# Optimization experiments

Hardware: AMD Instinct MI355X
Metric: run time of the kernel (lower is better)

## Reference

```python
import jax, jax.numpy as jnp
import numpy as np

D_MODEL = 1024
D_HIDDEN = 4096
NUM_BANKS = 16
NUM_SELECTED = 2


def setup_inputs() -> dict:
    key = jax.random.key(0)
    ks = jax.random.split(key, 7)
    s = 0.02
    return {
        "tensor": jax.random.normal(ks[0], (4, 1024, D_MODEL), dtype=jnp.float32),
        "Wr": jax.random.normal(ks[1], (D_MODEL, NUM_BANKS), dtype=jnp.float32) * s,
        "br": jnp.zeros((NUM_BANKS,), dtype=jnp.float32),
        "W1": jax.random.normal(ks[2], (NUM_BANKS, D_MODEL, D_HIDDEN), dtype=jnp.float32) * s,
        "b1": jnp.zeros((NUM_BANKS, D_HIDDEN), dtype=jnp.float32),
        "W2": jax.random.normal(ks[3], (NUM_BANKS, D_HIDDEN, D_MODEL), dtype=jnp.float32) * s,
        "b2": jnp.zeros((NUM_BANKS, D_MODEL), dtype=jnp.float32),
    }


def reference(tensor, Wr, br, W1, b1, W2, b2):
    # Router: softmax over banks, keep top-k probabilities (BankSelector)
    logits = jnp.einsum("bsd,de->bse", tensor, Wr) + br          # [B,S,E]
    probs = jax.nn.softmax(logits, axis=-1)
    topv, topi = jax.lax.top_k(probs, NUM_SELECTED)              # [B,S,K]
    # Dense gate [B,S,E]: selected banks carry their router probability,
    # all other banks are zeroed (equivalent to sparse dispatch/combine).
    gate = jnp.sum(jax.nn.one_hot(topi, NUM_BANKS, dtype=tensor.dtype)
                   * topv[..., None], axis=-2)                    # [B,S,E]
    # Banked expert FFN (BankedLinear x2 with ReLU between)
    h = jax.nn.relu(jnp.einsum("bsd,edh->bseh", tensor, W1) + b1)  # [B,S,E,Dh]
    y = jnp.einsum("bseh,ehm->bsem", h, W2) + b2                   # [B,S,E,Dm]
    # Weighted combine across selected banks
    out = jnp.einsum("bse,bsem->bsm", gate, y)                     # [B,S,Dm]
    return out
```

## Files before the change

### kernel.cpp

```cpp
#include <hip/hip_runtime.h>
#include <stdint.h>

#define D_MODEL   1024
#define D_HIDDEN  4096
#define NBANKS    16
#define NTOK      4096

#define BM 128
#define BN 128
#define BK 32
#define TBUF (BM * BK)
#define KS2 4
#define MAXT 512

typedef __attribute__((ext_vector_type(8))) short bf16x8;
typedef __attribute__((ext_vector_type(4))) float f32x4;
typedef __attribute__((ext_vector_type(4))) unsigned int u32x4;
typedef __attribute__((ext_vector_type(2))) unsigned int u32x2;

__device__ __forceinline__ unsigned short f2bf(float f) {
  unsigned u = __builtin_bit_cast(unsigned, f);
  u += 0x7FFFu + ((u >> 16) & 1u);
  return (unsigned short)(u >> 16);
}

__device__ __forceinline__ unsigned cvtpk(float lo, float hi) {
  unsigned r;
  asm("v_cvt_pk_bf16_f32 %0, %1, %2" : "=v"(r) : "v"(lo), "v"(hi));
  return r;
}

__device__ __forceinline__ void lds_barrier() {
  asm volatile("s_waitcnt lgkmcnt(0)" ::: "memory");
  __builtin_amdgcn_sched_barrier(0);
  __builtin_amdgcn_s_barrier();
  __builtin_amdgcn_sched_barrier(0);
}

__device__ __forceinline__ int sidx(int r, int k) {
  return (r << 5) + ((((k >> 3) ^ ((r >> 1) & 3)) << 3) | (k & 7));
}

__global__ __launch_bounds__(256) void zero_out_k(float4* __restrict__ out4,
                                                  int* __restrict__ counts) {
  size_t i = (size_t)blockIdx.x * 256 + threadIdx.x;
  out4[i] = make_float4(0.f, 0.f, 0.f, 0.f);
  if (blockIdx.x == 0 && threadIdx.x < NBANKS) counts[threadIdx.x] = 0;
}

__global__ __launch_bounds__(256) void cvtx_k(const float* __restrict__ X,
                                              unsigned short* __restrict__ Xb) {
  const size_t i = ((size_t)blockIdx.x * 256 + threadIdx.x) * 8;
  const float4 a = *(const float4*)(X + i);
  const float4 b = *(const float4*)(X + i + 4);
  u32x4 v;
  v[0] = cvtpk(a.x, a.y); v[1] = cvtpk(a.z, a.w);
  v[2] = cvtpk(b.x, b.y); v[3] = cvtpk(b.z, b.w);
  *(u32x4*)(Xb + i) = v;
}

__global__ __launch_bounds__(64) void router_k(const float* __restrict__ x,
                                               const float* __restrict__ Wr,
                                               const float* __restrict__ br,
                                               int* __restrict__ topIdx,
                                               float* __restrict__ topGate) {
  const int t = blockIdx.x;
  const int l = threadIdx.x;
  const float* xr = x + (size_t)t * D_MODEL;

  float acc[NBANKS];
#pragma unroll
  for (int e = 0; e < NBANKS; ++e) acc[e] = 0.f;

  for (int d = l; d < D_MODEL; d += 64) {
    const float xv = xr[d];
    const float* wrow = Wr + (size_t)d * NBANKS;
#pragma unroll
    for (int e = 0; e < NBANKS; ++e) acc[e] += xv * wrow[e];
  }
#pragma unroll
  for (int e = 0; e < NBANKS; ++e) {
#pragma unroll
    for (int m = 1; m < 64; m <<= 1) acc[e] += __shfl_xor(acc[e], m, 64);
  }
#pragma unroll
  for (int e = 0; e < NBANKS; ++e) acc[e] += br[e];

  if (l == 0) {
    float mx = acc[0];
#pragma unroll
    for (int e = 1; e < NBANKS; ++e) mx = fmaxf(mx, acc[e]);
    float p[NBANKS];
    float s = 0.f;
#pragma unroll
    for (int e = 0; e < NBANKS; ++e) { p[e] = expf(acc[e] - mx); s += p[e]; }
    int i0 = 0; float v0 = p[0];
#pragma unroll
    for (int e = 1; e < NBANKS; ++e) if (p[e] > v0) { v0 = p[e]; i0 = e; }
    int i1 = -1; float v1 = -1.f;
#pragma unroll
    for (int e = 0; e < NBANKS; ++e) if (e != i0 && p[e] > v1) { v1 = p[e]; i1 = e; }
    const float inv = 1.f / s;
    topIdx[2 * t]     = i0;
    topIdx[2 * t + 1] = i1;
    topGate[2 * t]     = v0 * inv;
    topGate[2 * t + 1] = v1 * inv;
  }
}

__global__ __launch_bounds__(256) void build_lists_k(const int* __restrict__ topIdx,
                                                     const float* __restrict__ topGate,
                                                     int* __restrict__ counts,
                                                     int* __restrict__ rowlist,
                                                     float* __restrict__ gatelist) {
  const int t = blockIdx.x * 256 + threadIdx.x;
  if (t >= NTOK) return;
#pragma unroll
  for (int k = 0; k < 2; ++k) {
    const int e = topIdx[2 * t + k];
    const int p = atomicAdd(&counts[e], 1);
    rowlist[e * NTOK + p]  = t;
    gatelist[e * NTOK + p] = topGate[2 * t + k];
  }
}

__global__ void scan_k(const int* __restrict__ counts, int* __restrict__ bankOff,
                       int* __restrict__ tileE, int* __restrict__ tileM,
                       int* __restrict__ nT) {
  if (threadIdx.x == 0) {
    int s = 0;
    int t = 0;
    for (int e = 0; e < NBANKS; ++e) {
      bankOff[e] = s;
      const int c = counts[e];
      s += c;
      for (int m = 0; m < c; m += BM) {
        tileE[t] = e;
        tileM[t] = m;
        ++t;
      }
    }
    bankOff[NBANKS] = s;
    nT[0] = t;
  }
}

__global__ __launch_bounds__(256, 2) void gemm1_k(const unsigned short* __restrict__ Xb,
                                                  const float* __restrict__ W1,
                                                  const float* __restrict__ b1,
                                                  const int* __restrict__ counts,
                                                  const int* __restrict__ bankOff,
                                                  const int* __restrict__ rowlist,
                                                  const int* __restrict__ tileE,
                                                  const int* __restrict__ tileM,
                                                  const int* __restrict__ nT,
                                                  unsigned short* __restrict__ H) {
  const int tI = blockIdx.y;
  if (tI >= nT[0]) return;
  const int e   = tileE[tI];
  const int m0  = tileM[tI];
  const int cnt = counts[e];
  const int n0  = blockIdx.x * BN;

  const int tid  = threadIdx.x;
  const int lane = tid & 63;
  const int w    = tid >> 6;
  const int wm   = (w >> 1) * 64;
  const int wn   = (w & 1) * 64;

  __shared__ unsigned short Xs[2 * TBUF];
  __shared__ unsigned short Ws[2 * TBUF];

  const int arow = tid >> 1;
  const int ak   = (tid & 1) * 16;
  const int gi   = min(m0 + arow, cnt - 1);
  const int tok  = rowlist[e * NTOK + gi];
  const unsigned short* Asrc = Xb + (size_t)tok * D_MODEL + ak;
  const int xo0 = sidx(arow, ak);
  const int xo1 = sidx(arow, ak + 8);

  const int n4 = 4 * (tid & 31);
  const int k4 = 4 * (tid >> 5);
  const float* Bsrc = W1 + (size_t)e * D_MODEL * D_HIDDEN + (size_t)k4 * D_HIDDEN + n0 + n4;
  int wo[4];
#pragma unroll
  for (int i = 0; i < 4; ++i) wo[i] = sidx(n4 + i, k4);

  const int fr = lane & 15;
  const int fc = (lane >> 4) * 8;
  int aoff[4], boff[4];
#pragma unroll
  for (int i = 0; i < 4; ++i) {
    aoff[i] = sidx(wm + i * 16 + fr, fc);
    boff[i] = sidx(wn + i * 16 + fr, fc);
  }

  bf16x8 pa0, pa1, qa0, qa1;
  float pb[4][4], qb[4][4];

  f32x4 acc[4][4];
#pragma unroll
  for (int i = 0; i < 4; ++i)
#pragma unroll
    for (int j = 0; j < 4; ++j)
#pragma unroll
      for (int r = 0; r < 4; ++r) acc[i][j][r] = 0.f;

  unsigned short* xc = &Xs[0];       unsigned short* wc = &Ws[0];
  unsigned short* xn = &Xs[TBUF];    unsigned short* wn_ = &Ws[TBUF];

  auto LOADP = [&](int t) {
    const unsigned short* ap = Asrc + t * BK;
    pa0 = *(const bf16x8*)(ap);
    pa1 = *(const bf16x8*)(ap + 8);
    const float* bp = Bsrc + (size_t)t * BK * D_HIDDEN;
#pragma unroll
    for (int kk = 0; kk < 4; ++kk)
      *(float4*)&pb[kk][0] = *(const float4*)(bp + (size_t)kk * D_HIDDEN);
  };
  auto LOADQ = [&](int t) {
    const unsigned short* ap = Asrc + t * BK;
    qa0 = *(const bf16x8*)(ap);
    qa1 = *(const bf16x8*)(ap + 8);
    const float* bp = Bsrc + (size_t)t * BK * D_HIDDEN;
#pragma unroll
    for (int kk = 0; kk < 4; ++kk)
      *(float4*)&qb[kk][0] = *(const float4*)(bp + (size_t)kk * D_HIDDEN);
  };
  auto WRITEP = [&](unsigned short* xs, unsigned short* ws) {
    *(bf16x8*)(xs + xo0) = pa0;
    *(bf16x8*)(xs + xo1) = pa1;
#pragma unroll
    for (int i = 0; i < 4; ++i) {
      u32x2 v;
      v[0] = cvtpk(pb[0][i], pb[1][i]);
      v[1] = cvtpk(pb[2][i], pb[3][i]);
      *(u32x2*)(ws + wo[i]) = v;
    }
  };
  auto WRITEQ = [&](unsigned short* xs, unsigned short* ws) {
    *(bf16x8*)(xs + xo0) = qa0;
    *(bf16x8*)(xs + xo1) = qa1;
#pragma unroll
    for (int i = 0; i < 4; ++i) {
      u32x2 v;
      v[0] = cvtpk(qb[0][i], qb[1][i]);
      v[1] = cvtpk(qb[2][i], qb[3][i]);
      *(u32x2*)(ws + wo[i]) = v;
    }
  };
  auto COMPUTE = [&](const unsigned short* xs, const unsigned short* ws) {
    bf16x8 af[4], bb[4];
#pragma unroll
    for (int mb = 0; mb < 4; ++mb) af[mb] = *(const bf16x8*)(xs + aoff[mb]);
#pragma unroll
    for (int nb = 0; nb < 4; ++nb) bb[nb] = *(const bf16x8*)(ws + boff[nb]);
#pragma unroll
    for (int mb = 0; mb < 4; ++mb)
#pragma unroll
      for (int nb = 0; nb < 4; ++nb)
        acc[mb][nb] = __builtin_amdgcn_mfma_f32_16x16x32_bf16(af[mb], bb[nb], acc[mb][nb], 0, 0, 0);
  };

  const int NT = D_MODEL / BK;
  LOADP(0);
  LOADQ(1);
  WRITEP(xc, wc);
  lds_barrier();
#pragma unroll 1
  for (int t = 0; t < NT; t += 2) {
    if (t + 2 < NT) LOADP(t + 2);
    __builtin_amdgcn_sched_barrier(0);
    COMPUTE(xc, wc);
    WRITEQ(xn, wn_);
    lds_barrier();
    if (t + 3 < NT) LOADQ(t + 3);
    __builtin_amdgcn_sched_barrier(0);
    COMPUTE(xn, wn_);
    if (t + 2 < NT) WRITEP(xc, wc);
    lds_barrier();
  }

  const int hb = bankOff[e] + m0;
  const int rq = (lane >> 4) * 4;
#pragma unroll
  for (int nb = 0; nb < 4; ++nb) {
    const int col = n0 + wn + nb * 16 + fr;
    const float bias = b1[e * D_HIDDEN + col];
#pragma unroll
    for (int mb = 0; mb < 4; ++mb)
#pragma unroll
      for (int r = 0; r < 4; ++r) {
        const int rowT = wm + mb * 16 + rq + r;
        if (m0 + rowT < cnt) {
          float v = acc[mb][nb][r] + bias;
          v = fmaxf(v, 0.f);
          H[(size_t)(hb + rowT) * D_HIDDEN + col] = f2bf(v);
        }
      }
  }
}

__global__ __launch_bounds__(256, 2) void gemm2_k(const unsigned short* __restrict__ H,
                                                  const float* __restrict__ W2,
                                                  const float* __restrict__ b2,
                                                  const int* __restrict__ counts,
                                                  const int* __restrict__ bankOff,
                                                  const int* __restrict__ rowlist,
                                                  const float* __restrict__ gatelist,
                                                  const int* __restrict__ tileE,
                                                  const int* __restrict__ tileM,
                                                  const int* __restrict__ nT,
                                                  float* __restrict__ out) {
  const int tI = blockIdx.y >> 2;
  const int kc = blockIdx.y & 3;
  if (tI >= nT[0]) return;
  const int e   = tileE[tI];
  const int m0  = tileM[tI];
  const int cnt = counts[e];
  const int n0  = blockIdx.x * BN;
  const int kc0 = kc * (D_HIDDEN / KS2);

  const int tid  = threadIdx.x;
  const int lane = tid & 63;
  const int w    = tid >> 6;
  const int wm   = (w >> 1) * 64;
  const int wn   = (w & 1) * 64;

  __shared__ unsigned short Xs[2 * TBUF];
  __shared__ unsigned short Ws[2 * TBUF];

  const int arow = tid >> 1;
  const int ak   = (tid & 1) * 16;
  const int hb   = bankOff[e];
  const int gi   = hb + min(m0 + arow, cnt - 1);
  const unsigned short* Asrc = H + (size_t)gi * D_HIDDEN + kc0 + ak;
  const int xo0 = sidx(arow, ak);
  const int xo1 = sidx(arow, ak + 8);

  const int n4 = 4 * (tid & 31);
  const int k4 = 4 * (tid >> 5);
  const float* Bsrc = W2 + (size_t)e * D_HIDDEN * D_MODEL + (size_t)(kc0 + k4) * D_MODEL + n0 + n4;
  int wo[4];
#pragma unroll
  for (int i = 0; i < 4; ++i) wo[i] = sidx(n4 + i, k4);

  const int fr = lane & 15;
  const int fc = (lane >> 4) * 8;
  int aoff[4], boff[4];
#pragma unroll
  for (int i = 0; i < 4; ++i) {
    aoff[i] = sidx(wm + i * 16 + fr, fc);
    boff[i] = sidx(wn + i * 16 + fr, fc);
  }

  bf16x8 pa0, pa1, qa0, qa1;
  float pb[4][4], qb[4][4];

  f32x4 acc[4][4];
#pragma unroll
  for (int i = 0; i < 4; ++i)
#pragma unroll
    for (int j = 0; j < 4; ++j)
#pragma unroll
      for (int r = 0; r < 4; ++r) acc[i][j][r] = 0.f;

  unsigned short* xc = &Xs[0];       unsigned short* wc = &Ws[0];
  unsigned short* xn = &Xs[TBUF];    unsigned short* wn_ = &Ws[TBUF];

  auto LOADP = [&](int t) {
    const unsigned short* ap = Asrc + t * BK;
    pa0 = *(const bf16x8*)(ap);
    pa1 = *(const bf16x8*)(ap + 8);
    const float* bp = Bsrc + (size_t)t * BK * D_MODEL;
#pragma unroll
    for (int kk = 0; kk < 4; ++kk)
      *(float4*)&pb[kk][0] = *(const float4*)(bp + (size_t)kk * D_MODEL);
  };
  auto LOADQ = [&](int t) {
    const unsigned short* ap = Asrc + t * BK;
    qa0 = *(const bf16x8*)(ap);
    qa1 = *(const bf16x8*)(ap + 8);
    const float* bp = Bsrc + (size_t)t * BK * D_MODEL;
#pragma unroll
    for (int kk = 0; kk < 4; ++kk)
      *(float4*)&qb[kk][0] = *(const float4*)(bp + (size_t)kk * D_MODEL);
  };
  auto WRITEP = [&](unsigned short* xs, unsigned short* ws) {
    *(bf16x8*)(xs + xo0) = pa0;
    *(bf16x8*)(xs + xo1) = pa1;
#pragma unroll
    for (int i = 0; i < 4; ++i) {
      u32x2 v;
      v[0] = cvtpk(pb[0][i], pb[1][i]);
      v[1] = cvtpk(pb[2][i], pb[3][i]);
      *(u32x2*)(ws + wo[i]) = v;
    }
  };
  auto WRITEQ = [&](unsigned short* xs, unsigned short* ws) {
    *(bf16x8*)(xs + xo0) = qa0;
    *(bf16x8*)(xs + xo1) = qa1;
#pragma unroll
    for (int i = 0; i < 4; ++i) {
      u32x2 v;
      v[0] = cvtpk(qb[0][i], qb[1][i]);
      v[1] = cvtpk(qb[2][i], qb[3][i]);
      *(u32x2*)(ws + wo[i]) = v;
    }
  };
  auto COMPUTE = [&](const unsigned short* xs, const unsigned short* ws) {
    bf16x8 af[4], bb[4];
#pragma unroll
    for (int mb = 0; mb < 4; ++mb) af[mb] = *(const bf16x8*)(xs + aoff[mb]);
#pragma unroll
    for (int nb = 0; nb < 4; ++nb) bb[nb] = *(const bf16x8*)(ws + boff[nb]);
#pragma unroll
    for (int mb = 0; mb < 4; ++mb)
#pragma unroll
      for (int nb = 0; nb < 4; ++nb)
        acc[mb][nb] = __builtin_amdgcn_mfma_f32_16x16x32_bf16(af[mb], bb[nb], acc[mb][nb], 0, 0, 0);
  };

  const int NT = (D_HIDDEN / KS2) / BK;
  LOADP(0);
  LOADQ(1);
  WRITEP(xc, wc);
  lds_barrier();
#pragma unroll 1
  for (int t = 0; t < NT; t += 2) {
    if (t + 2 < NT) LOADP(t + 2);
    __builtin_amdgcn_sched_barrier(0);
    COMPUTE(xc, wc);
    WRITEQ(xn, wn_);
    lds_barrier();
    if (t + 3 < NT) LOADQ(t + 3);
    __builtin_amdgcn_sched_barrier(0);
    COMPUTE(xn, wn_);
    if (t + 2 < NT) WRITEP(xc, wc);
    lds_barrier();
  }

  const int rq = (lane >> 4) * 4;
  float bias[4];
#pragma unroll
  for (int nb = 0; nb < 4; ++nb)
    bias[nb] = (kc == 0) ? b2[e * D_MODEL + n0 + wn + nb * 16 + fr] : 0.f;

#pragma unroll
  for (int mb = 0; mb < 4; ++mb)
#pragma unroll
    for (int r = 0; r < 4; ++r) {
      const int rowT = wm + mb * 16 + rq + r;
      if (m0 + rowT < cnt) {
        const int si = e * NTOK + m0 + rowT;
        const int tok = rowlist[si];
        const float g = gatelist[si];
        float* orow = out + (size_t)tok * D_MODEL;
#pragma unroll
        for (int nb = 0; nb < 4; ++nb) {
          const int col = n0 + wn + nb * 16 + fr;
          atomicAdd(&orow[col], g * (acc[mb][nb][r] + bias[nb]));
        }
      }
    }
}

extern "C" void kernel_launch(void* const* d_in, const int* in_sizes, int n_in,
                              void* d_out, int out_size, void* d_ws, size_t ws_size,
                              hipStream_t stream) {
  const float* X  = (const float*)d_in[0];
  const float* Wr = (const float*)d_in[1];
  const float* br = (const float*)d_in[2];
  const float* W1 = (const float*)d_in[3];
  const float* b1 = (const float*)d_in[4];
  const float* W2 = (const float*)d_in[5];
  const float* b2 = (const float*)d_in[6];
  float* out = (float*)d_out;

  char* w = (char*)d_ws;
  int*   topIdx   = (int*)(w);
  float* topGate  = (float*)(w + (32 << 10));
  int*   counts   = (int*)(w + (64 << 10));
  int*   bankOff  = (int*)(w + (64 << 10) + 256);
  int*   rowlist  = (int*)(w + (66 << 10));
  float* gatelist = (float*)(w + (66 << 10) + NBANKS * NTOK * 4);
  int*   tileE    = (int*)(w + (600 << 10));
  int*   tileM    = (int*)(w + (604 << 10));
  int*   nT       = (int*)(w + (608 << 10));
  unsigned short* Xb = (unsigned short*)(w + (1 << 20));
  unsigned short* H  = (unsigned short*)(w + (16 << 20));

  const size_t needed = (size_t)(16 << 20) + (size_t)(NTOK * 2) * D_HIDDEN * 2;
  if (ws_size < needed) return;

  zero_out_k<<<dim3(4096), dim3(256), 0, stream>>>((float4*)out, counts);
  cvtx_k<<<dim3(NTOK * D_MODEL / 8 / 256), dim3(256), 0, stream>>>(X, Xb);
  router_k<<<dim3(NTOK), dim3(64), 0, stream>>>(X, Wr, br, topIdx, topGate);
  build_lists_k<<<dim3(16), dim3(256), 0, stream>>>(topIdx, topGate, counts, rowlist, gatelist);
  scan_k<<<dim3(1), dim3(64), 0, stream>>>(counts, bankOff, tileE, tileM, nT);
  gemm1_k<<<dim3(D_HIDDEN / BN, MAXT), dim3(256), 0, stream>>>(
      Xb, W1, b1, counts, bankOff, rowlist, tileE, tileM, nT, H);
  gemm2_k<<<dim3(D_MODEL / BN, MAXT * KS2), dim3(256), 0, stream>>>(
      H, W2, b2, counts, bankOff, rowlist, gatelist, tileE, tileM, nT, out);
}
```

Measured before the change: 447.8 us.

## Use scalar strided weight loads, halve gemm2 split-K, raise occupancy bounds

Each thread now loads weight elements as scalars with a stride of 32 columns instead of one float4 covering four adjacent columns. The intent is that LDS writes of the transposed bf16 tiles land in different banks and avoid conflicts, at the cost of more global load instructions, though each wavefront's loads still coalesce. The gemm2 split-K factor drops from 4 to 2, which halves the atomic or partial-sum traffic into the output but leaves fewer blocks. Launch bounds rise to 4 blocks per SM, which caps register use and may cause spills given the large accumulator and prefetch arrays.

```diff
diff --git a/kernel.cpp b/kernel.cpp
--- a/kernel.cpp
+++ b/kernel.cpp
@@ -10,7 +10,7 @@
 #define BN 128
 #define BK 32
 #define TBUF (BM * BK)
-#define KS2 4
+#define KS2 2
 #define MAXT 512
 
 typedef __attribute__((ext_vector_type(8))) short bf16x8;
@@ -145,7 +145,7 @@
   }
 }
 
-__global__ __launch_bounds__(256, 2) void gemm1_k(const unsigned short* __restrict__ Xb,
+__global__ __launch_bounds__(256, 4) void gemm1_k(const unsigned short* __restrict__ Xb,
                                                   const float* __restrict__ W1,
                                                   const float* __restrict__ b1,
                                                   const int* __restrict__ counts,
@@ -179,12 +179,12 @@
   const int xo0 = sidx(arow, ak);
   const int xo1 = sidx(arow, ak + 8);
 
-  const int n4 = 4 * (tid & 31);
-  const int k4 = 4 * (tid >> 5);
-  const float* Bsrc = W1 + (size_t)e * D_MODEL * D_HIDDEN + (size_t)k4 * D_HIDDEN + n0 + n4;
+  const int bm  = tid & 31;
+  const int bk4 = 4 * (tid >> 5);
+  const float* Bsrc = W1 + (size_t)e * D_MODEL * D_HIDDEN + (size_t)bk4 * D_HIDDEN + n0 + bm;
   int wo[4];
 #pragma unroll
-  for (int i = 0; i < 4; ++i) wo[i] = sidx(n4 + i, k4);
+  for (int j = 0; j < 4; ++j) wo[j] = sidx(bm + 32 * j, bk4);
 
   const int fr = lane & 15;
   const int fc = (lane >> 4) * 8;
@@ -215,8 +215,10 @@
     pa1 = *(const bf16x8*)(ap + 8);
     const float* bp = Bsrc + (size_t)t * BK * D_HIDDEN;
 #pragma unroll
-    for (int kk = 0; kk < 4; ++kk)
-      *(float4*)&pb[kk][0] = *(const float4*)(bp + (size_t)kk * D_HIDDEN);
+    for (int j = 0; j < 4; ++j)
+#pragma unroll
+      for (int kk = 0; kk < 4; ++kk)
+        pb[j][kk] = bp[(size_t)kk * D_HIDDEN + 32 * j];
   };
   auto LOADQ = [&](int t) {
     const unsigned short* ap = Asrc + t * BK;
@@ -224,29 +226,31 @@
     qa1 = *(const bf16x8*)(ap + 8);
     const float* bp = Bsrc + (size_t)t * BK * D_HIDDEN;
 #pragma unroll
-    for (int kk = 0; kk < 4; ++kk)
-      *(float4*)&qb[kk][0] = *(const float4*)(bp + (size_t)kk * D_HIDDEN);
+    for (int j = 0; j < 4; ++j)
+#pragma unroll
+      for (int kk = 0; kk < 4; ++kk)
+        qb[j][kk] = bp[(size_t)kk * D_HIDDEN + 32 * j];
   };
   auto WRITEP = [&](unsigned short* xs, unsigned short* ws) {
     *(bf16x8*)(xs + xo0) = pa0;
     *(bf16x8*)(xs + xo1) = pa1;
 #pragma unroll
-    for (int i = 0; i < 4; ++i) {
+    for (int j = 0; j < 4; ++j) {
       u32x2 v;
-      v[0] = cvtpk(pb[0][i], pb[1][i]);
-      v[1] = cvtpk(pb[2][i], pb[3][i]);
-      *(u32x2*)(ws + wo[i]) = v;
+      v[0] = cvtpk(pb[j][0], pb[j][1]);
+      v[1] = cvtpk(pb[j][2], pb[j][3]);
+      *(u32x2*)(ws + wo[j]) = v;
     }
   };
   auto WRITEQ = [&](unsigned short* xs, unsigned short* ws) {
     *(bf16x8*)(xs + xo0) = qa0;
     *(bf16x8*)(xs + xo1) = qa1;
 #pragma unroll
-    for (int i = 0; i < 4; ++i) {
+    for (int j = 0; j < 4; ++j) {
       u32x2 v;
-      v[0] = cvtpk(qb[0][i], qb[1][i]);
-      v[1] = cvtpk(qb[2][i], qb[3][i]);
-      *(u32x2*)(ws + wo[i]) = v;
+      v[0] = cvtpk(qb[j][0], qb[j][1]);
+      v[1] = cvtpk(qb[j][2], qb[j][3]);
+      *(u32x2*)(ws + wo[j]) = v;
     }
   };
   auto COMPUTE = [&](const unsigned short* xs, const unsigned short* ws) {
@@ -301,7 +305,7 @@
   }
 }
 
-__global__ __launch_bounds__(256, 2) void gemm2_k(const unsigned short* __restrict__ H,
+__global__ __launch_bounds__(256, 4) void gemm2_k(const unsigned short* __restrict__ H,
                                                   const float* __restrict__ W2,
                                                   const float* __restrict__ b2,
                                                   const int* __restrict__ counts,
@@ -312,8 +316,8 @@
                                                   const int* __restrict__ tileM,
                                                   const int* __restrict__ nT,
                                                   float* __restrict__ out) {
-  const int tI = blockIdx.y >> 2;
-  const int kc = blockIdx.y & 3;
+  const int tI = blockIdx.y >> 1;
+  const int kc = blockIdx.y & 1;
   if (tI >= nT[0]) return;
   const int e   = tileE[tI];
   const int m0  = tileM[tI];
@@ -338,12 +342,12 @@
   const int xo0 = sidx(arow, ak);
   const int xo1 = sidx(arow, ak + 8);
 
-  const int n4 = 4 * (tid & 31);
-  const int k4 = 4 * (tid >> 5);
-  const float* Bsrc = W2 + (size_t)e * D_HIDDEN * D_MODEL + (size_t)(kc0 + k4) * D_MODEL + n0 + n4;
+  const int bm  = tid & 31;
+  const int bk4 = 4 * (tid >> 5);
+  const float* Bsrc = W2 + (size_t)e * D_HIDDEN * D_MODEL + (size_t)(kc0 + bk4) * D_MODEL + n0 + bm;
   int wo[4];
 #pragma unroll
-  for (int i = 0; i < 4; ++i) wo[i] = sidx(n4 + i, k4);
+  for (int j = 0; j < 4; ++j) wo[j] = sidx(bm + 32 * j, bk4);
 
   const int fr = lane & 15;
   const int fc = (lane >> 4) * 8;
@@ -374,8 +378,10 @@
     pa1 = *(const bf16x8*)(ap + 8);
     const float* bp = Bsrc + (size_t)t * BK * D_MODEL;
 #pragma unroll
-    for (int kk = 0; kk < 4; ++kk)
-      *(float4*)&pb[kk][0] = *(const float4*)(bp + (size_t)kk * D_MODEL);
+    for (int j = 0; j < 4; ++j)
+#pragma unroll
+      for (int kk = 0; kk < 4; ++kk)
+        pb[j][kk] = bp[(size_t)kk * D_MODEL + 32 * j];
   };
   auto LOADQ = [&](int t) {
     const unsigned short* ap = Asrc + t * BK;
@@ -383,29 +389,31 @@
     qa1 = *(const bf16x8*)(ap + 8);
     const float* bp = Bsrc + (size_t)t * BK * D_MODEL;
 #pragma unroll
-    for (int kk = 0; kk < 4; ++kk)
-      *(float4*)&qb[kk][0] = *(const float4*)(bp + (size_t)kk * D_MODEL);
+    for (int j = 0; j < 4; ++j)
+#pragma unroll
+      for (int kk = 0; kk < 4; ++kk)
+        qb[j][kk] = bp[(size_t)kk * D_MODEL + 32 * j];
   };
   auto WRITEP = [&](unsigned short* xs, unsigned short* ws) {
     *(bf16x8*)(xs + xo0) = pa0;
     *(bf16x8*)(xs + xo1) = pa1;
 #pragma unroll
-    for (int i = 0; i < 4; ++i) {
+    for (int j = 0; j < 4; ++j) {
       u32x2 v;
-      v[0] = cvtpk(pb[0][i], pb[1][i]);
-      v[1] = cvtpk(pb[2][i], pb[3][i]);
-      *(u32x2*)(ws + wo[i]) = v;
+      v[0] = cvtpk(pb[j][0], pb[j][1]);
+      v[1] = cvtpk(pb[j][2], pb[j][3]);
+      *(u32x2*)(ws + wo[j]) = v;
     }
   };
   auto WRITEQ = [&](unsigned short* xs, unsigned short* ws) {
     *(bf16x8*)(xs + xo0) = qa0;
     *(bf16x8*)(xs + xo1) = qa1;
 #pragma unroll
-    for (int i = 0; i < 4; ++i) {
+    for (int j = 0; j < 4; ++j) {
       u32x2 v;
-      v[0] = cvtpk(qb[0][i], qb[1][i]);
-      v[1] = cvtpk(qb[2][i], qb[3][i]);
-      *(u32x2*)(ws + wo[i]) = v;
+      v[0] = cvtpk(qb[j][0], qb[j][1]);
+      v[1] = cvtpk(qb[j][2], qb[j][3]);
+      *(u32x2*)(ws + wo[j]) = v;
     }
   };
   auto COMPUTE = [&](const unsigned short* xs, const unsigned short* ws) {
```

Result: slower. 975.3 us (+117.8%).
